# Optimization experiments

Hardware: AMD Instinct MI355X
Metric: run time of the kernel (lower is better)

Reference implementation:

```python
import jax, jax.numpy as jnp
import numpy as np

N, DEG, NFEAT, NHID, NHEADS, NCLASS = 50000, 32, 512, 64, 8, 40
ALPHA = 0.2  # LeakyReLU negative slope


def _xavier(key, shape, gain=1.414):
    fan_in, fan_out = shape[-2], shape[-1]
    std = gain * np.sqrt(2.0 / (fan_in + fan_out))
    return (jax.random.normal(key, shape, dtype=jnp.float32) * std).astype(jnp.float32)


def setup_inputs() -> dict:
    key = jax.random.key(0)
    ks = jax.random.split(key, 9)
    E = N * DEG
    src = jax.random.randint(ks[0], (E,), 0, N, dtype=jnp.int32)
    dst = jax.random.randint(ks[1], (E,), 0, N, dtype=jnp.int32)
    loop = jnp.arange(N, dtype=jnp.int32)  # self-loops ensure nonzero rowsums
    edge = jnp.stack([jnp.concatenate([src, loop]), jnp.concatenate([dst, loop])])
    x = jax.random.normal(ks[2], (N, NFEAT), dtype=jnp.float32)
    return {
        "x": x,
        "edge": edge,  # [2, E+N] COO indices (row=target, col=source)
        "W": _xavier(ks[3], (NHEADS, NFEAT, NHID)),
        "W_pair": _xavier(ks[4], (NHEADS, 2 * NHID, NHID)),
        "a": _xavier(ks[5], (NHEADS, NHID, 1))[..., 0],  # [H, NHID]
        "W_out": _xavier(ks[6], (NHEADS * NHID, NCLASS)),
        "W_pair_out": _xavier(ks[7], (2 * NCLASS, NCLASS)),
        "a_out": _xavier(ks[8], (NCLASS, 1))[..., 0],  # [NCLASS]
    }


def _att_layer(x, src, dst, W, W_pair, a, concat):
    n = x.shape[0]
    d = W.shape[1]
    h = x @ W  # [N, d]
    # cat(h_src, h_dst) @ W_pair == h_src @ W_pair[:d] + h_dst @ W_pair[d:]
    z = jax.nn.leaky_relu(h[src] @ W_pair[:d] + h[dst] @ W_pair[d:], ALPHA)  # [E, d]
    e = jnp.exp(z @ a)  # [E]
    rowsum = jax.ops.segment_sum(e, src, num_segments=n)  # A @ ones
    h_prime = jax.ops.segment_sum(e[:, None] * h[dst], src, num_segments=n)  # A @ h
    h_prime = h_prime / rowsum[:, None]
    return jax.nn.elu(h_prime) if concat else h_prime


def reference(x, edge, W, W_pair, a, W_out, W_pair_out, a_out):
    src, dst = edge[0], edge[1]
    heads = [_att_layer(x, src, dst, W[i], W_pair[i], a[i], True) for i in range(NHEADS)]
    x2 = jax.nn.elu(jnp.concatenate(heads, axis=1))  # [N, H*NHID]
    out = jax.nn.elu(_att_layer(x2, src, dst, W_out, W_pair_out, a_out, False))
    return out  # [N, NCLASS]
```

## Files before the change

kernel.cpp:

```cpp
#include <hip/hip_runtime.h>
#include <hip/hip_bf16.h>
#include <hip/hip_fp16.h>

typedef _Float16 f16;
typedef _Float16 f16x2 __attribute__((ext_vector_type(2)));
typedef _Float16 f16x8 __attribute__((ext_vector_type(8)));
typedef float f32x4 __attribute__((ext_vector_type(4)));

#define HEADS 8
#define HID 64
#define NCLS 40
#define FEAT 512

__global__ void pack_Wh(const float* __restrict__ W, f16* __restrict__ Wt) {
    int idx = blockIdx.x * blockDim.x + threadIdx.x;
    if (idx >= 512 * 512) return;
    int c = idx >> 9, k = idx & 511;
    Wt[idx] = (f16)W[(c >> 6) * 512 * 64 + k * 64 + (c & 63)];
}

__global__ void pack_Bp(const float* __restrict__ Wp, f16* __restrict__ Bt) {
    int idx = blockIdx.x * blockDim.x + threadIdx.x;
    if (idx >= 8 * 128 * 64) return;
    int head = idx >> 13, c = (idx >> 6) & 127, k = idx & 63;
    Bt[idx] = (f16)Wp[head * 8192 + ((c >> 6) * 64 + k) * 64 + (c & 63)];
}

__global__ void pack_Wo(const float* __restrict__ Wo, f16* __restrict__ Wt) {
    int idx = blockIdx.x * blockDim.x + threadIdx.x;
    if (idx >= 40 * 512) return;
    int c = idx >> 9, k = idx & 511;
    Wt[idx] = (f16)Wo[k * 40 + c];
}

__global__ void repack_wpo(const float* __restrict__ Wpo, float* __restrict__ B2p) {
    int idx = blockIdx.x * blockDim.x + threadIdx.x;
    if (idx >= 40 * 80) return;
    int k = idx / 80;
    int c = idx % 80;
    int p = c / 40;
    int j = c % 40;
    B2p[idx] = Wpo[(p * 40 + k) * 40 + j];
}

__global__ void pack_vh2(const float* __restrict__ h2, const float* __restrict__ uv2,
                         f16x2* __restrict__ vh2, int total) {
    int i = blockIdx.x * blockDim.x + threadIdx.x;
    if (i >= total) return;
    int t = i / 40, k = i % 40;
    vh2[i] = f16x2{(f16)uv2[(size_t)t * 80 + 40 + k], (f16)h2[i]};
}

__global__ void hist_kernel(const int* __restrict__ src, int* __restrict__ counts, int ne) {
    int i = blockIdx.x * blockDim.x + threadIdx.x;
    int stride = gridDim.x * blockDim.x;
    for (; i < ne; i += stride) atomicAdd(&counts[src[i]], 1);
}

__global__ void scan_partial(const int* __restrict__ counts, int* __restrict__ partial, int n) {
    __shared__ int s[256];
    int i = blockIdx.x * 256 + threadIdx.x;
    s[threadIdx.x] = (i < n) ? counts[i] : 0;
    __syncthreads();
    for (int d = 128; d > 0; d >>= 1) {
        if (threadIdx.x < d) s[threadIdx.x] += s[threadIdx.x + d];
        __syncthreads();
    }
    if (threadIdx.x == 0) partial[blockIdx.x] = s[0];
}

__global__ void scan_top(int* __restrict__ partial, int nb) {
    __shared__ int s[1024];
    int tid = threadIdx.x;
    s[tid] = (tid < nb) ? partial[tid] : 0;
    __syncthreads();
    for (int d = 1; d < 1024; d <<= 1) {
        int v = (tid >= d) ? s[tid - d] : 0;
        __syncthreads();
        s[tid] += v;
        __syncthreads();
    }
    if (tid < nb) partial[tid] = (tid == 0) ? 0 : s[tid - 1];
}

__global__ void scan_final(const int* __restrict__ counts, const int* __restrict__ partialEx,
                           int* __restrict__ offsets, int* __restrict__ cursor, int n) {
    __shared__ int s[256];
    int i = blockIdx.x * 256 + threadIdx.x;
    int v = (i < n) ? counts[i] : 0;
    s[threadIdx.x] = v;
    __syncthreads();
    for (int d = 1; d < 256; d <<= 1) {
        int u = (threadIdx.x >= d) ? s[threadIdx.x - d] : 0;
        __syncthreads();
        s[threadIdx.x] += u;
        __syncthreads();
    }
    int excl = partialEx[blockIdx.x] + s[threadIdx.x] - v;
    if (i < n) {
        cursor[i] = excl;
        offsets[i] = excl;
        if (i == n - 1) offsets[n] = excl + v;
    }
}

__global__ void scatter_kernel(const int* __restrict__ src, const int* __restrict__ dst,
                               int* __restrict__ cursor, int* __restrict__ dsts, int ne) {
    int i = blockIdx.x * blockDim.x + threadIdx.x;
    int stride = gridDim.x * blockDim.x;
    for (; i < ne; i += stride) {
        int pos = atomicAdd(&cursor[src[i]], 1);
        dsts[pos] = dst[i];
    }
}

__global__ void sort_dsts(const int* __restrict__ offsets, int* __restrict__ dsts, int n) {
    int wave = threadIdx.x >> 6, lane = threadIdx.x & 63;
    int t = blockIdx.x * (blockDim.x >> 6) + wave;
    if (t >= n) return;
    int s0 = offsets[t], s1 = offsets[t + 1];
    for (int base = s0; base < s1; base += 64) {
        int cnt = s1 - base;
        if (cnt > 64) cnt = 64;
        int v = (lane < cnt) ? dsts[base + lane] : 0x7fffffff;
#pragma unroll
        for (int k = 2; k <= 64; k <<= 1) {
#pragma unroll
            for (int j = k >> 1; j > 0; j >>= 1) {
                int o = __shfl_xor(v, j, 64);
                bool lower = (lane & j) == 0;
                bool asc = (lane & k) == 0;
                int mn = min(v, o), mx = max(v, o);
                v = (lower == asc) ? mn : mx;
            }
        }
        if (lane < cnt) dsts[base + lane] = v;
    }
}

__device__ __forceinline__ void stC(float* p, float v) { *p = v; }
__device__ __forceinline__ void stC(f16* p, float v) { *p = (f16)v; }
__device__ __forceinline__ f16x8 ldA8(const f16* p) { return *(const f16x8*)p; }
__device__ __forceinline__ f16x8 ldA8(const float* p) {
    float4 a = ((const float4*)p)[0];
    float4 b = ((const float4*)p)[1];
    f16x8 r = {(f16)a.x, (f16)a.y, (f16)a.z, (f16)a.w, (f16)b.x, (f16)b.y, (f16)b.z, (f16)b.w};
    return r;
}

template <typename AT, typename CT>
__global__ __launch_bounds__(256)
void gemm_mfma(const AT* __restrict__ A, int lda, int acol0, int acolStride,
               const f16* __restrict__ Bt, long bBatchStride, int K,
               CT* __restrict__ C, int ldc, int ccolStride,
               int nrows, int ncols) {
    __shared__ f16 As[128][40];
    __shared__ f16 Bs[128][40];
    const int batch = blockIdx.y;
    const int row0 = blockIdx.x * 128;
    const int col0 = blockIdx.z * 128;
    const int a0 = acol0 + batch * acolStride;
    const f16* Bb = Bt + (size_t)batch * bBatchStride;
    const int tid = threadIdx.x;
    const int lane = tid & 63;
    const int wave = tid >> 6;
    const int wr = (wave >> 1) * 64;
    const int wc = (wave & 1) * 64;
    f32x4 acc[4][4] = {};

    for (int k0 = 0; k0 < K; k0 += 32) {
#pragma unroll
        for (int i = 0; i < 2; i++) {
            int idx = tid + i * 256;
            int r = idx >> 2, ch = idx & 3;
            int gr = row0 + r;
            f16x8 val = {};
            if (gr < nrows) val = ldA8(A + (size_t)gr * lda + a0 + k0 + ch * 8);
            *(f16x8*)(&As[r][ch * 8]) = val;
        }
#pragma unroll
        for (int i = 0; i < 2; i++) {
            int idx = tid + i * 256;
            int r = idx >> 2, ch = idx & 3;
            int gc = col0 + r;
            f16x8 val = {};
            if (gc < ncols) val = *(const f16x8*)(Bb + (size_t)gc * K + k0 + ch * 8);
            *(f16x8*)(&Bs[r][ch * 8]) = val;
        }
        __syncthreads();
        f16x8 af[4], bf[4];
#pragma unroll
        for (int t = 0; t < 4; t++)
            af[t] = *(const f16x8*)(&As[wr + t * 16 + (lane & 15)][(lane >> 4) * 8]);
#pragma unroll
        for (int t = 0; t < 4; t++)
            bf[t] = *(const f16x8*)(&Bs[wc + t * 16 + (lane & 15)][(lane >> 4) * 8]);
#pragma unroll
        for (int i = 0; i < 4; i++)
#pragma unroll
            for (int j = 0; j < 4; j++)
                acc[i][j] = __builtin_amdgcn_mfma_f32_16x16x32_f16(af[i], bf[j], acc[i][j], 0, 0, 0);
        __syncthreads();
    }
    const int crow = (lane >> 4) * 4;
    const int ccol = lane & 15;
#pragma unroll
    for (int i = 0; i < 4; i++) {
#pragma unroll
        for (int j = 0; j < 4; j++) {
            int gc = col0 + wc + j * 16 + ccol;
            if (gc >= ncols) continue;
#pragma unroll
            for (int r = 0; r < 4; r++) {
                int gr = row0 + wr + i * 16 + crow + r;
                if (gr < nrows)
                    stC(&C[(size_t)gr * ldc + (size_t)batch * ccolStride + gc], acc[i][j][r]);
            }
        }
    }
}

__global__ void gemm_kernel(const float* __restrict__ A, int lda,
                            const float* __restrict__ B, int ldb,
                            float* __restrict__ C, int ldc,
                            int nrows, int K, int ncols) {
    __shared__ __align__(16) float As[16][68];
    __shared__ __align__(16) float Bs[16][64];
    const int colblk = blockIdx.z * 64;
    const int row0 = blockIdx.x * 64;
    const int tid = threadIdx.x;
    const int tm = tid >> 4, tn = tid & 15;
    float acc[4][4] = {};
    for (int k0 = 0; k0 < K; k0 += 16) {
#pragma unroll
        for (int i = 0; i < 4; i++) {
            int idx = tid + i * 256;
            int m = idx >> 4;
            int k = idx & 15;
            int gr = row0 + m;
            float v = 0.f;
            if (gr < nrows && (k0 + k) < K) v = A[(size_t)gr * lda + k0 + k];
            As[k][m] = v;
        }
#pragma unroll
        for (int i = 0; i < 4; i++) {
            int idx = tid + i * 256;
            int k = idx >> 6;
            int j = idx & 63;
            float v = 0.f;
            if ((k0 + k) < K && (colblk + j) < ncols) v = B[(size_t)(k0 + k) * ldb + colblk + j];
            Bs[k][j] = v;
        }
        __syncthreads();
#pragma unroll
        for (int k = 0; k < 16; k++) {
            float av[4], bv[4];
#pragma unroll
            for (int i = 0; i < 4; i++) av[i] = As[k][tm * 4 + i];
#pragma unroll
            for (int j = 0; j < 4; j++) bv[j] = Bs[k][tn * 4 + j];
#pragma unroll
            for (int i = 0; i < 4; i++)
#pragma unroll
                for (int j = 0; j < 4; j++) acc[i][j] += av[i] * bv[j];
        }
        __syncthreads();
    }
#pragma unroll
    for (int i = 0; i < 4; i++) {
        int gr = row0 + tm * 4 + i;
        if (gr >= nrows) continue;
#pragma unroll
        for (int j = 0; j < 4; j++) {
            int gc = colblk + tn * 4 + j;
            if (gc < ncols) C[(size_t)gr * ldc + gc] = acc[i][j];
        }
    }
}

__device__ __forceinline__ void store8h(f16* p, const float o[8]) {
    f16x8 v;
#pragma unroll
    for (int k = 0; k < 8; k++) v[k] = (f16)o[k];
    *(f16x8*)p = v;
}

__device__ __forceinline__ float dot8_lrelu(const uint4& vr, const f16x2 u2[4],
                                            const f16x2 a2[4]) {
    const f16x2* vp = (const f16x2*)&vr;
    float p = 0.f;
#pragma unroll
    for (int k = 0; k < 4; k++) {
        f16x2 w = u2[k] + vp[k];
        f16x2 lr = __builtin_elementwise_max(w, w * (_Float16)0.2f);
#if __has_builtin(__builtin_amdgcn_fdot2)
        p = __builtin_amdgcn_fdot2(lr, a2[k], p, false);
#else
        p = fmaf((float)lr[0], (float)a2[k][0], p);
        p = fmaf((float)lr[1], (float)a2[k][1], p);
#endif
    }
    return p;
}

__global__ void edge_l1(const int* __restrict__ offsets, const int* __restrict__ dsts,
                        const f16* __restrict__ h, const f16* __restrict__ uv,
                        const float* __restrict__ a, f16* __restrict__ x2, int n) {
    const int lane = threadIdx.x & 63;
    const int wave = threadIdx.x >> 6;
    const int t = blockIdx.x * (blockDim.x >> 6) + wave;
    if (t >= n) return;
    const int head = lane >> 3;
    const int sub = lane & 7;
    const unsigned voff = head * 128 + 64 + sub * 8;
    const unsigned uoff = head * 128 + sub * 8;
    const unsigned hoff = lane * 8;

    f16x2 u2[4], a2[4];
    {
        uint4 ur = *(const uint4*)(uv + (size_t)t * 1024 + uoff);
        const f16x2* up = (const f16x2*)&ur;
#pragma unroll
        for (int k = 0; k < 4; k++) u2[k] = up[k];
        const float4* ap = (const float4*)(a + hoff);
        float4 a0 = ap[0], a1 = ap[1];
        a2[0] = f16x2{(f16)a0.x, (f16)a0.y};
        a2[1] = f16x2{(f16)a0.z, (f16)a0.w};
        a2[2] = f16x2{(f16)a1.x, (f16)a1.y};
        a2[3] = f16x2{(f16)a1.z, (f16)a1.w};
    }

    const int s0 = offsets[t], s1 = offsets[t + 1];
    float acc[8] = {0.f, 0.f, 0.f, 0.f, 0.f, 0.f, 0.f, 0.f};
    float rs = 0.f;

    for (int base = s0; base < s1; base += 64) {
        int cnt = s1 - base;
        if (cnt > 64) cnt = 64;
        int myd = (lane < cnt) ? dsts[base + lane] : 0;
        int d0 = __shfl(myd, 0, 64);
        uint4 vr = *(const uint4*)(uv + (size_t)(unsigned)d0 * 1024 + voff);
        uint4 hr = *(const uint4*)(h + (size_t)(unsigned)d0 * 512 + hoff);
        for (int j = 0; j < cnt; j++) {
            uint4 vr_n, hr_n;
            if (j + 1 < cnt) {
                int dn = __shfl(myd, j + 1, 64);
                vr_n = *(const uint4*)(uv + (size_t)(unsigned)dn * 1024 + voff);
                hr_n = *(const uint4*)(h + (size_t)(unsigned)dn * 512 + hoff);
            }
            float p = dot8_lrelu(vr, u2, a2);
            p += __shfl_xor(p, 1, 64);
            p += __shfl_xor(p, 2, 64);
            p += __shfl_xor(p, 4, 64);
            float wgt = __expf(p);
            rs += wgt;
            const f16* hp = (const f16*)&hr;
#pragma unroll
            for (int k = 0; k < 8; k++) acc[k] = fmaf(wgt, (float)hp[k], acc[k]);
            vr = vr_n;
            hr = hr_n;
        }
    }
    float inv = 1.f / rs;
    float o[8];
#pragma unroll
    for (int k = 0; k < 8; k++) {
        float hp = acc[k] * inv;
        float e1 = hp > 0.f ? hp : expm1f(hp);
        o[k] = e1 > 0.f ? e1 : expm1f(e1);
    }
    store8h(x2 + (size_t)t * 512 + hoff, o);
}

__global__ void edge_l2(const int* __restrict__ offsets, const int* __restrict__ dsts,
                        const f16x2* __restrict__ vh2, const float* __restrict__ uv2,
                        const float* __restrict__ a_out, float* __restrict__ out, int n) {
    int wave = threadIdx.x >> 6;
    int lane = threadIdx.x & 63;
    int t = blockIdx.x * (blockDim.x >> 6) + wave;
    if (t >= n) return;
    bool act = lane < 40;
    float u_t = act ? uv2[(size_t)t * 80 + lane] : 0.f;
    float a_l = act ? a_out[lane] : 0.f;
    int s0 = offsets[t], s1 = offsets[t + 1];
    float acc = 0.f, rs = 0.f;
    const f16x2 z2 = {(_Float16)0.f, (_Float16)0.f};
    for (int base = s0; base < s1; base += 64) {
        int cnt = s1 - base;
        if (cnt > 64) cnt = 64;
        int myd = (lane < cnt) ? dsts[base + lane] : 0;
        int d0 = __shfl(myd, 0, 64);
        f16x2 vh0 = act ? vh2[(size_t)(unsigned)d0 * 40 + lane] : z2;
        for (int j = 0; j < cnt; j++) {
            f16x2 vh1 = z2;
            if (j + 1 < cnt) {
                int dn = __shfl(myd, j + 1, 64);
                vh1 = act ? vh2[(size_t)(unsigned)dn * 40 + lane] : z2;
            }
            float w = u_t + (float)vh0[0];
            float lr = fmaxf(w, 0.2f * w);
            float p = a_l * lr;
#pragma unroll
            for (int m = 32; m; m >>= 1) p += __shfl_xor(p, m, 64);
            float wgt = __expf(p);
            rs += wgt;
            acc = fmaf(wgt, (float)vh0[1], acc);
            vh0 = vh1;
        }
    }
    if (act) {
        float hp = acc / rs;
        out[(size_t)t * 40 + lane] = hp > 0.f ? hp : expm1f(hp);
    }
}

extern "C" void kernel_launch(void* const* d_in, const int* in_sizes, int n_in,
                              void* d_out, int out_size, void* d_ws, size_t ws_size,
                              hipStream_t stream) {
    const float* x         = (const float*)d_in[0];
    const int*   edge      = (const int*)d_in[1];
    const float* W         = (const float*)d_in[2];
    const float* W_pair    = (const float*)d_in[3];
    const float* a         = (const float*)d_in[4];
    const float* W_out     = (const float*)d_in[5];
    const float* W_pair_out= (const float*)d_in[6];
    const float* a_out     = (const float*)d_in[7];
    float* out = (float*)d_out;

    const int n  = in_sizes[0] / FEAT;
    const int ne = in_sizes[1] / 2;
    const int* srcArr = edge;
    const int* dstArr = edge + ne;

    char* ws = (char*)d_ws;
    size_t off = 0;
    auto alloc = [&](size_t bytes) -> void* {
        void* p = ws + off;
        off = (off + bytes + 255) & ~(size_t)255;
        return p;
    };
    f16* h    = (f16*)alloc((size_t)n * 512 * sizeof(f16));
    f16* uv   = (f16*)alloc((size_t)n * 1024 * sizeof(f16));
    f16* x2   = (f16*)alloc((size_t)n * 512 * sizeof(f16));
    f16x2* vh2 = (f16x2*)alloc((size_t)n * 40 * sizeof(f16x2));
    f16* Wh_t = (f16*)alloc(512 * 512 * sizeof(f16));
    f16* Bp_t = (f16*)alloc(8 * 128 * 64 * sizeof(f16));
    f16* Wo_t = (f16*)alloc(40 * 512 * sizeof(f16));
    float* B2p = (float*)alloc(40 * 80 * sizeof(float));
    int* counts  = (int*)alloc((size_t)n * sizeof(int));
    int* offsets = (int*)alloc((size_t)(n + 1) * sizeof(int));
    int* cursor  = (int*)alloc((size_t)n * sizeof(int));
    int* partial = (int*)alloc(1024 * sizeof(int));
    int* dsts    = (int*)alloc((size_t)ne * sizeof(int));
    float* h2  = (float*)h;
    float* uv2 = (float*)((char*)h + (size_t)n * 40 * sizeof(float));

    const int nb = (n + 255) / 256;

    hipMemsetAsync(counts, 0, (size_t)n * sizeof(int), stream);
    hist_kernel<<<2048, 256, 0, stream>>>(srcArr, counts, ne);
    scan_partial<<<nb, 256, 0, stream>>>(counts, partial, n);
    scan_top<<<1, 1024, 0, stream>>>(partial, nb);
    scan_final<<<nb, 256, 0, stream>>>(counts, partial, offsets, cursor, n);
    scatter_kernel<<<2048, 256, 0, stream>>>(srcArr, dstArr, cursor, dsts, ne);
    sort_dsts<<<(n + 3) / 4, 256, 0, stream>>>(offsets, dsts, n);

    pack_Wh<<<(512 * 512 + 255) / 256, 256, 0, stream>>>(W, Wh_t);
    pack_Bp<<<(8 * 128 * 64 + 255) / 256, 256, 0, stream>>>(W_pair, Bp_t);
    pack_Wo<<<(40 * 512 + 255) / 256, 256, 0, stream>>>(W_out, Wo_t);
    repack_wpo<<<(40 * 80 + 255) / 256, 256, 0, stream>>>(W_pair_out, B2p);

    const int mBlocks = (n + 127) / 128;

    gemm_mfma<float, f16><<<dim3(mBlocks, 1, 4), 256, 0, stream>>>(
        x, 512, 0, 0, Wh_t, 0, 512, h, 512, 0, n, 512);

    gemm_mfma<f16, f16><<<dim3(mBlocks, 8, 1), 256, 0, stream>>>(
        h, 512, 0, 64, Bp_t, 128L * 64, 64, uv, 1024, 128, n, 128);

    edge_l1<<<dim3((n + 3) / 4), 256, 0, stream>>>(offsets, dsts, h, uv, a, x2, n);

    gemm_mfma<f16, float><<<dim3(mBlocks, 1, 1), 256, 0, stream>>>(
        x2, 512, 0, 0, Wo_t, 0, 512, h2, 40, 0, n, 40);

    gemm_kernel<<<dim3((n + 63) / 64, 1, 2), 256, 0, stream>>>(
        h2, 40, B2p, 80, uv2, 80, n, 40, 80);

    pack_vh2<<<(n * 40 + 255) / 256, 256, 0, stream>>>(h2, uv2, vh2, n * 40);

    edge_l2<<<dim3((n + 3) / 4), 256, 0, stream>>>(offsets, dsts, vh2, uv2, a_out, out, n);
}
```

Baseline: 1.063 ms.

## Merge weight packing kernels, drop neighbor sort, process 8 edges per wave in layer 2

Fuses four small weight-packing kernels into a single launch and removes the per-node bitonic sort of destination indices. The layer-2 edge kernel is restructured so each wave handles 8 edges at once, with 8 lanes per edge each covering 5 classes. This replaces the serial per-edge full-wave reduction and gives more gather parallelism. Dropping the sort makes the order of summation depend on scatter atomics, so results may differ slightly from run to run, and layer-1 gathers lose locality.

Measured after the change: 925.9 us. 1.15x faster.

```diff
diff --git a/kernel.cpp b/kernel.cpp
--- a/kernel.cpp
+++ b/kernel.cpp
@@ -12,35 +12,28 @@
 #define NCLS 40
 #define FEAT 512
 
-__global__ void pack_Wh(const float* __restrict__ W, f16* __restrict__ Wt) {
+__global__ void pack_all(const float* __restrict__ W, const float* __restrict__ Wp,
+                         const float* __restrict__ Wo, const float* __restrict__ Wpo,
+                         f16* __restrict__ Wh_t, f16* __restrict__ Bp_t,
+                         f16* __restrict__ Wo_t, float* __restrict__ B2p) {
     int idx = blockIdx.x * blockDim.x + threadIdx.x;
-    if (idx >= 512 * 512) return;
-    int c = idx >> 9, k = idx & 511;
-    Wt[idx] = (f16)W[(c >> 6) * 512 * 64 + k * 64 + (c & 63)];
-}
-
-__global__ void pack_Bp(const float* __restrict__ Wp, f16* __restrict__ Bt) {
-    int idx = blockIdx.x * blockDim.x + threadIdx.x;
-    if (idx >= 8 * 128 * 64) return;
-    int head = idx >> 13, c = (idx >> 6) & 127, k = idx & 63;
-    Bt[idx] = (f16)Wp[head * 8192 + ((c >> 6) * 64 + k) * 64 + (c & 63)];
-}
-
-__global__ void pack_Wo(const float* __restrict__ Wo, f16* __restrict__ Wt) {
-    int idx = blockIdx.x * blockDim.x + threadIdx.x;
-    if (idx >= 40 * 512) return;
-    int c = idx >> 9, k = idx & 511;
-    Wt[idx] = (f16)Wo[k * 40 + c];
-}
-
-__global__ void repack_wpo(const float* __restrict__ Wpo, float* __restrict__ B2p) {
-    int idx = blockIdx.x * blockDim.x + threadIdx.x;
-    if (idx >= 40 * 80) return;
-    int k = idx / 80;
-    int c = idx % 80;
-    int p = c / 40;
-    int j = c % 40;
-    B2p[idx] = Wpo[(p * 40 + k) * 40 + j];
+    if (idx < 512 * 512) {
+        int c = idx >> 9, k = idx & 511;
+        Wh_t[idx] = (f16)W[(c >> 6) * 512 * 64 + k * 64 + (c & 63)];
+    } else if (idx < 512 * 512 + 8 * 128 * 64) {
+        int i = idx - 512 * 512;
+        int head = i >> 13, c = (i >> 6) & 127, k = i & 63;
+        Bp_t[i] = (f16)Wp[head * 8192 + ((c >> 6) * 64 + k) * 64 + (c & 63)];
+    } else if (idx < 512 * 512 + 8 * 128 * 64 + 40 * 512) {
+        int i = idx - (512 * 512 + 8 * 128 * 64);
+        int c = i >> 9, k = i & 511;
+        Wo_t[i] = (f16)Wo[k * 40 + c];
+    } else if (idx < 512 * 512 + 8 * 128 * 64 + 40 * 512 + 40 * 80) {
+        int i = idx - (512 * 512 + 8 * 128 * 64 + 40 * 512);
+        int k = i / 80, c = i % 80;
+        int p = c / 40, j = c % 40;
+        B2p[i] = Wpo[(p * 40 + k) * 40 + j];
+    }
 }
 
 __global__ void pack_vh2(const float* __restrict__ h2, const float* __restrict__ uv2,
@@ -111,30 +104,6 @@
     for (; i < ne; i += stride) {
         int pos = atomicAdd(&cursor[src[i]], 1);
         dsts[pos] = dst[i];
-    }
-}
-
-__global__ void sort_dsts(const int* __restrict__ offsets, int* __restrict__ dsts, int n) {
-    int wave = threadIdx.x >> 6, lane = threadIdx.x & 63;
-    int t = blockIdx.x * (blockDim.x >> 6) + wave;
-    if (t >= n) return;
-    int s0 = offsets[t], s1 = offsets[t + 1];
-    for (int base = s0; base < s1; base += 64) {
-        int cnt = s1 - base;
-        if (cnt > 64) cnt = 64;
-        int v = (lane < cnt) ? dsts[base + lane] : 0x7fffffff;
-#pragma unroll
-        for (int k = 2; k <= 64; k <<= 1) {
-#pragma unroll
-            for (int j = k >> 1; j > 0; j >>= 1) {
-                int o = __shfl_xor(v, j, 64);
-                bool lower = (lane & j) == 0;
-                bool asc = (lane & k) == 0;
-                int mn = min(v, o), mx = max(v, o);
-                v = (lower == asc) ? mn : mx;
-            }
-        }
-        if (lane < cnt) dsts[base + lane] = v;
     }
 }
 
@@ -375,42 +344,64 @@
 __global__ void edge_l2(const int* __restrict__ offsets, const int* __restrict__ dsts,
                         const f16x2* __restrict__ vh2, const float* __restrict__ uv2,
                         const float* __restrict__ a_out, float* __restrict__ out, int n) {
-    int wave = threadIdx.x >> 6;
-    int lane = threadIdx.x & 63;
-    int t = blockIdx.x * (blockDim.x >> 6) + wave;
+    const int lane = threadIdx.x & 63;
+    const int wave = threadIdx.x >> 6;
+    const int t = blockIdx.x * (blockDim.x >> 6) + wave;
     if (t >= n) return;
-    bool act = lane < 40;
-    float u_t = act ? uv2[(size_t)t * 80 + lane] : 0.f;
-    float a_l = act ? a_out[lane] : 0.f;
-    int s0 = offsets[t], s1 = offsets[t + 1];
-    float acc = 0.f, rs = 0.f;
-    const f16x2 z2 = {(_Float16)0.f, (_Float16)0.f};
+    const int g = lane >> 3;
+    const int s = lane & 7;
+    float u5[5], a5[5];
+#pragma unroll
+    for (int k = 0; k < 5; k++) {
+        u5[k] = uv2[(size_t)t * 80 + s * 5 + k];
+        a5[k] = a_out[s * 5 + k];
+    }
+    const int s0 = offsets[t], s1 = offsets[t + 1];
+    float acc[5] = {0.f, 0.f, 0.f, 0.f, 0.f};
+    float rs = 0.f;
     for (int base = s0; base < s1; base += 64) {
         int cnt = s1 - base;
         if (cnt > 64) cnt = 64;
         int myd = (lane < cnt) ? dsts[base + lane] : 0;
-        int d0 = __shfl(myd, 0, 64);
-        f16x2 vh0 = act ? vh2[(size_t)(unsigned)d0 * 40 + lane] : z2;
-        for (int j = 0; j < cnt; j++) {
-            f16x2 vh1 = z2;
-            if (j + 1 < cnt) {
-                int dn = __shfl(myd, j + 1, 64);
-                vh1 = act ? vh2[(size_t)(unsigned)dn * 40 + lane] : z2;
+        for (int j8 = 0; j8 < cnt; j8 += 8) {
+            int eidx = j8 + g;
+            bool active = eidx < cnt;
+            int d = __shfl(myd, active ? eidx : 0, 64);
+            f16x2 vh[5];
+            const f16x2* vp = vh2 + (size_t)(unsigned)d * 40 + s * 5;
+#pragma unroll
+            for (int k = 0; k < 5; k++) vh[k] = vp[k];
+            float p = 0.f;
+#pragma unroll
+            for (int k = 0; k < 5; k++) {
+                float w = u5[k] + (float)vh[k][0];
+                p = fmaf(a5[k], fmaxf(w, 0.2f * w), p);
             }
-            float w = u_t + (float)vh0[0];
-            float lr = fmaxf(w, 0.2f * w);
-            float p = a_l * lr;
-#pragma unroll
-            for (int m = 32; m; m >>= 1) p += __shfl_xor(p, m, 64);
-            float wgt = __expf(p);
+            p += __shfl_xor(p, 1, 64);
+            p += __shfl_xor(p, 2, 64);
+            p += __shfl_xor(p, 4, 64);
+            float wgt = active ? __expf(p) : 0.f;
             rs += wgt;
-            acc = fmaf(wgt, (float)vh0[1], acc);
-            vh0 = vh1;
-        }
-    }
-    if (act) {
-        float hp = acc / rs;
-        out[(size_t)t * 40 + lane] = hp > 0.f ? hp : expm1f(hp);
+#pragma unroll
+            for (int k = 0; k < 5; k++) acc[k] = fmaf(wgt, (float)vh[k][1], acc[k]);
+        }
+    }
+    rs += __shfl_xor(rs, 8, 64);
+    rs += __shfl_xor(rs, 16, 64);
+    rs += __shfl_xor(rs, 32, 64);
+#pragma unroll
+    for (int k = 0; k < 5; k++) {
+        acc[k] += __shfl_xor(acc[k], 8, 64);
+        acc[k] += __shfl_xor(acc[k], 16, 64);
+        acc[k] += __shfl_xor(acc[k], 32, 64);
+    }
+    if (g == 0) {
+        float inv = 1.f / rs;
+#pragma unroll
+        for (int k = 0; k < 5; k++) {
+            float hp = acc[k] * inv;
+            out[(size_t)t * 40 + s * 5 + k] = hp > 0.f ? hp : expm1f(hp);
+        }
     }
 }
 
@@ -463,12 +454,10 @@
     scan_top<<<1, 1024, 0, stream>>>(partial, nb);
     scan_final<<<nb, 256, 0, stream>>>(counts, partial, offsets, cursor, n);
     scatter_kernel<<<2048, 256, 0, stream>>>(srcArr, dstArr, cursor, dsts, ne);
-    sort_dsts<<<(n + 3) / 4, 256, 0, stream>>>(offsets, dsts, n);
-
-    pack_Wh<<<(512 * 512 + 255) / 256, 256, 0, stream>>>(W, Wh_t);
-    pack_Bp<<<(8 * 128 * 64 + 255) / 256, 256, 0, stream>>>(W_pair, Bp_t);
-    pack_Wo<<<(40 * 512 + 255) / 256, 256, 0, stream>>>(W_out, Wo_t);
-    repack_wpo<<<(40 * 80 + 255) / 256, 256, 0, stream>>>(W_pair_out, B2p);
+
+    const int packTotal = 512 * 512 + 8 * 128 * 64 + 40 * 512 + 40 * 80;
+    pack_all<<<(packTotal + 255) / 256, 256, 0, stream>>>(
+        W, W_pair, W_out, W_pair_out, Wh_t, Bp_t, Wo_t, B2p);
 
     const int mBlocks = (n + 127) / 128;
 
```
